# Performance work log

Measured on AMD Instinct MI355X. Metric: run time of the kernel, lower is better.

The kernel has to match this reference:

```python
import jax, jax.numpy as jnp
import numpy as np

N_NODES = 100000
N_EDGES = 1600000
IN_C = 64
HID = 64


def _glorot(key, shape):
    fan_in, fan_out = shape[1], shape[0]
    lim = (6.0 / (fan_in + fan_out)) ** 0.5
    return jax.random.uniform(key, shape, jnp.float32, -lim, lim)


def setup_inputs() -> dict:
    key = jax.random.key(0)
    ks = jax.random.split(key, 8)
    x = jax.random.normal(ks[0], (N_NODES, IN_C), jnp.float32)
    edge_index = jax.random.randint(ks[1], (2, N_EDGES), 0, N_NODES, jnp.int32)
    return {
        "x": x,
        "edge_index": edge_index,
        # conv1 (SAGEConv in->hid): lin_l (bias), lin_r (no bias)
        "W1l": _glorot(ks[2], (HID, IN_C)),
        "b1l": jnp.zeros((HID,), jnp.float32),
        "W1r": _glorot(ks[3], (HID, IN_C)),
        # conv2 (SAGEConv hid->hid)
        "W2l": _glorot(ks[4], (HID, HID)),
        "b2l": jnp.zeros((HID,), jnp.float32),
        "W2r": _glorot(ks[5], (HID, HID)),
        # edge scorer: Linear(2*hid, 1)
        "Wlin": _glorot(ks[6], (1, 2 * HID)),
        "blin": jnp.zeros((1,), jnp.float32),
    }


def _sage_conv(x, src, dst, Wl, bl, Wr, n_nodes):
    # mean aggregation of source features onto destination nodes
    agg = jax.ops.segment_sum(x[src], dst, num_segments=n_nodes)  # [N, F]
    cnt = jax.ops.segment_sum(jnp.ones((src.shape[0],), x.dtype), dst,
                              num_segments=n_nodes)  # [N]
    mean = agg / jnp.maximum(cnt, 1.0)[:, None]  # isolated nodes -> 0
    return mean @ Wl.T + bl + x @ Wr.T


def reference(x, edge_index, W1l, b1l, W1r, W2l, b2l, W2r, Wlin, blin):
    src, dst = edge_index[0], edge_index[1]
    n = x.shape[0]
    h = jax.nn.relu(_sage_conv(x, src, dst, W1l, b1l, W1r, n))
    h = jax.nn.relu(_sage_conv(h, src, dst, W2l, b2l, W2r, n))
    he = jnp.concatenate([h[src], h[dst]], axis=1)  # [E, 2*HID]
    return (he @ Wlin.T + blin).squeeze(-1)  # [E]
```

## Files before the change

kernel.cpp:

```cpp
#include <hip/hip_runtime.h>
#include <hip/hip_bf16.h>

#define N_NODES 100000
#define N_EDGES 1600000
#define NBUCK 196
#define BCAP 12288
#define CHUNK 4096
#define PART_BLOCKS 391
#define MSTRIDE 36


typedef __hip_bfloat16 bf16;
typedef short short8 __attribute__((ext_vector_type(8)));
typedef float f32x4 __attribute__((ext_vector_type(4)));
typedef unsigned int uint;

__device__ __forceinline__ short f2bs(float f) {
    bf16 h = __float2bfloat16(f);
    short s; __builtin_memcpy(&s, &h, 2); return s;
}
__device__ __forceinline__ float lo_bf(uint w) {
    uint v = w << 16; float f; __builtin_memcpy(&f, &v, 4); return f;
}
__device__ __forceinline__ float hi_bf(uint w) {
    uint v = w & 0xFFFF0000u; float f; __builtin_memcpy(&f, &v, 4); return f;
}
__device__ __forceinline__ uint pack2(float a, float b) {
    return (uint)(unsigned short)f2bs(a) | ((uint)(unsigned short)f2bs(b) << 16);
}
__device__ __forceinline__ short8 load8bf(const bf16* __restrict__ p, long idx) {
    return *(const short8*)((const short*)p + idx);
}

__global__ __launch_bounds__(256) void convert_kernel(
    const float* __restrict__ in, bf16* __restrict__ out, int* __restrict__ gcur,
    const float* __restrict__ W1l, const float* __restrict__ W1r,
    const float* __restrict__ W2l, const float* __restrict__ W2r,
    bf16* __restrict__ wb)
{
    if (blockIdx.x < 6250) {
        int i = blockIdx.x * 256 + threadIdx.x;
        float4 v = ((const float4*)in)[i];
        uint2 o;
        o.x = pack2(v.x, v.y);
        o.y = pack2(v.z, v.w);
        ((uint2*)out)[i] = o;
        if (blockIdx.x == 0) gcur[threadIdx.x] = threadIdx.x * BCAP;
    } else {
        for (int k = threadIdx.x; k < 16384; k += 256) {
            float v;
            if (k < 4096)       v = W1l[k];
            else if (k < 8192)  v = W1r[k - 4096];
            else if (k < 12288) v = W2l[k - 8192];
            else                v = W2r[k - 12288];
            wb[k] = __float2bfloat16(v);
        }
    }
}


__global__ __launch_bounds__(256) void partition_kernel(
    const int* __restrict__ src, const int* __restrict__ dst,
    int* __restrict__ gcur, int* __restrict__ pk)
{
    __shared__ int h[256], scn[256], cur[256], gb[256];
    __shared__ int pl[CHUNK];
    __shared__ unsigned char bb[CHUNK];
    int t = threadIdx.x;
    h[t] = 0;
    __syncthreads();
    int e0 = blockIdx.x * CHUNK;
    for (int i = t; i < CHUNK; i += 256) {
        int e = e0 + i;
        if (e < N_EDGES) atomicAdd(&h[dst[e] >> 9], 1);
    }
    __syncthreads();
    if (t < 64) {
        int v0 = h[t * 4], v1 = h[t * 4 + 1], v2 = h[t * 4 + 2], v3 = h[t * 4 + 3];
        int i0 = v0, i1 = i0 + v1, i2 = i1 + v2, i3 = i2 + v3;
        int run = i3;
#pragma unroll
        for (int off = 1; off < 64; off <<= 1) {
            int u = __shfl_up(run, off);
            if (t >= off) run += u;
        }
        int excl = run - i3;
        scn[t * 4]     = excl + i0;
        scn[t * 4 + 1] = excl + i1;
        scn[t * 4 + 2] = excl + i2;
        scn[t * 4 + 3] = excl + i3;
    }
    __syncthreads();
    cur[t] = scn[t] - h[t];
    __syncthreads();
    int cnt_local = scn[255];
    for (int i = t; i < CHUNK; i += 256) {
        int e = e0 + i;
        if (e < N_EDGES) {
            int d = dst[e];
            int b = d >> 9;
            int p = atomicAdd(&cur[b], 1);
            pl[p] = src[e] | ((d & 511) << 17);
            bb[p] = (unsigned char)b;
        }
    }
    __syncthreads();
    if (h[t] > 0) gb[t] = atomicAdd(&gcur[t], h[t]);
    __syncthreads();
    for (int i = t; i < cnt_local; i += 256) {
        int b = bb[i];
        int pos = gb[b] + (i - (scn[b] - h[b]));
        if (pos < (b + 1) * BCAP) pk[pos] = pl[i];
    }
}

__global__ __launch_bounds__(512) void csr_build(
    const int* __restrict__ gcur, const int* __restrict__ pk,
    int* __restrict__ csr, int2* __restrict__ node_range)
{
    __shared__ int deg[512], scn[512], cur[512];
    __shared__ int csr_l[BCAP];
    int t = threadIdx.x;
    int b = blockIdx.x;
    int base = b * BCAP;
    int cnt = gcur[b] - base;
    if (cnt > BCAP) cnt = BCAP;
    deg[t] = 0;
    __syncthreads();
    for (int i = t; i < cnt; i += 512)
        atomicAdd(&deg[pk[base + i] >> 17], 1);
    __syncthreads();
    if (t < 64) {
        int e[8], inc[8], s = 0;
#pragma unroll
        for (int k = 0; k < 8; k++) { e[k] = deg[t * 8 + k]; s += e[k]; inc[k] = s; }
        int run = s;
#pragma unroll
        for (int off = 1; off < 64; off <<= 1) {
            int u = __shfl_up(run, off);
            if (t >= off) run += u;
        }
        int excl = run - s;
#pragma unroll
        for (int k = 0; k < 8; k++) scn[t * 8 + k] = excl + inc[k];
    }
    __syncthreads();
    int excl = scn[t] - deg[t];
    cur[t] = excl;
    int n = (b << 9) + t;
    if (n < N_NODES) node_range[n] = make_int2(base + excl, base + excl + deg[t]);
    __syncthreads();
    for (int i = t; i < cnt; i += 512) {
        int v = pk[base + i];
        int p = atomicAdd(&cur[v >> 17], 1);
        csr_l[p] = v & 0x1FFFF;
    }
    __syncthreads();
    for (int i = t; i < cnt; i += 512)
        csr[base + i] = csr_l[i];
}


__device__ __forceinline__ void gather_mean_lds(
    const bf16* __restrict__ feat, const int2* __restrict__ node_range,
    const int* __restrict__ csr, int nb0, uint* __restrict__ mean_l)
{
    int wave = threadIdx.x >> 6, lane = threadIdx.x & 63;
    int g = lane >> 3, ci = lane & 7;
    int nl = wave * 8 + g;
    int n = nb0 + nl;
    int2 rg = (n < N_NODES) ? node_range[n] : make_int2(0, 0);
    int beg = rg.x, end = rg.y;
    const uint* fw = (const uint*)feat;
    float a0 = 0.f, a1 = 0.f, a2 = 0.f, a3 = 0.f;
    float a4 = 0.f, a5 = 0.f, a6 = 0.f, a7 = 0.f;
    int i = beg;
    for (; i + 3 < end; i += 4) {
        int s0 = csr[i], s1 = csr[i + 1], s2 = csr[i + 2], s3 = csr[i + 3];
        uint4 w0 = *(const uint4*)(fw + (long)s0 * 32 + ci * 4);
        uint4 w1 = *(const uint4*)(fw + (long)s1 * 32 + ci * 4);
        uint4 w2 = *(const uint4*)(fw + (long)s2 * 32 + ci * 4);
        uint4 w3 = *(const uint4*)(fw + (long)s3 * 32 + ci * 4);
        a0 += lo_bf(w0.x) + lo_bf(w1.x) + lo_bf(w2.x) + lo_bf(w3.x);
        a1 += hi_bf(w0.x) + hi_bf(w1.x) + hi_bf(w2.x) + hi_bf(w3.x);
        a2 += lo_bf(w0.y) + lo_bf(w1.y) + lo_bf(w2.y) + lo_bf(w3.y);
        a3 += hi_bf(w0.y) + hi_bf(w1.y) + hi_bf(w2.y) + hi_bf(w3.y);
        a4 += lo_bf(w0.z) + lo_bf(w1.z) + lo_bf(w2.z) + lo_bf(w3.z);
        a5 += hi_bf(w0.z) + hi_bf(w1.z) + hi_bf(w2.z) + hi_bf(w3.z);
        a6 += lo_bf(w0.w) + lo_bf(w1.w) + lo_bf(w2.w) + lo_bf(w3.w);
        a7 += hi_bf(w0.w) + hi_bf(w1.w) + hi_bf(w2.w) + hi_bf(w3.w);
    }
    for (; i < end; i++) {
        int s = csr[i];
        uint4 w = *(const uint4*)(fw + (long)s * 32 + ci * 4);
        a0 += lo_bf(w.x); a1 += hi_bf(w.x);
        a2 += lo_bf(w.y); a3 += hi_bf(w.y);
        a4 += lo_bf(w.z); a5 += hi_bf(w.z);
        a6 += lo_bf(w.w); a7 += hi_bf(w.w);
    }
    int d = end - beg;
    float inv = d > 0 ? 1.0f / (float)d : 0.0f;
    uint4 q;
    q.x = pack2(a0 * inv, a1 * inv);
    q.y = pack2(a2 * inv, a3 * inv);
    q.z = pack2(a4 * inv, a5 * inv);
    q.w = pack2(a6 * inv, a7 * inv);
    *(uint4*)(mean_l + nl * MSTRIDE + ci * 4) = q;
}

__device__ __forceinline__ short8 load_bfrag(
    const bf16* __restrict__ wlb, int f, int c, int quad)
{
    if (c < 2) return load8bf(wlb, (long)f * 64 + c * 32 + quad * 8);
    return load8bf(wlb, 4096 + (long)f * 64 + (c - 2) * 32 + quad * 8);
}

__global__ __launch_bounds__(512) void layer1_fused(
    const bf16* __restrict__ xb, const int2* __restrict__ nrng,
    const int* __restrict__ csr, const bf16* __restrict__ wlb,
    const float* __restrict__ bl, bf16* __restrict__ h_out)
{
    __shared__ uint mean_l[64 * MSTRIDE];
    int nb0 = blockIdx.x * 64;
    gather_mean_lds(xb, nrng, csr, nb0, mean_l);
    __syncthreads();
    int tid = threadIdx.x;
    int wave = tid >> 6, lane = tid & 63;
    if (wave >= 4) return;
    int quad = lane >> 4, n16 = lane & 15;
    int nb = nb0 + wave * 16;
    int ln = wave * 16 + n16;

    int node_a = nb + n16;
    int na = node_a < N_NODES ? node_a : N_NODES - 1;
    short8 a[4];
#pragma unroll
    for (int c = 0; c < 2; c++)
        a[c] = *(const short8*)(mean_l + ln * MSTRIDE + c * 16 + quad * 4);
#pragma unroll
    for (int c = 0; c < 2; c++)
        a[2 + c] = load8bf(xb, (long)na * 64 + c * 32 + quad * 8);

#pragma unroll
    for (int t = 0; t < 4; t++) {
        int f = 16 * t + n16;
        f32x4 acc = {0.f, 0.f, 0.f, 0.f};
#pragma unroll
        for (int c = 0; c < 4; c++) {
            short8 b = load_bfrag(wlb, f, c, quad);
            acc = __builtin_amdgcn_mfma_f32_16x16x32_bf16(a[c], b, acc, 0, 0, 0);
        }
        float bias = bl[f];
#pragma unroll
        for (int r = 0; r < 4; r++) {
            int node = nb + quad * 4 + r;
            if (node < N_NODES)
                h_out[(long)node * 64 + f] = __float2bfloat16(fmaxf(acc[r] + bias, 0.0f));
        }
    }
}

__global__ __launch_bounds__(512) void layer2_fused(
    const bf16* __restrict__ h1, const int2* __restrict__ nrng,
    const int* __restrict__ csr, const bf16* __restrict__ wlb,
    const float* __restrict__ bl, const float* __restrict__ Wlin,
    float* __restrict__ s_src, float* __restrict__ s_dst)
{
    __shared__ uint mean_l[64 * MSTRIDE];
    int nb0 = blockIdx.x * 64;
    gather_mean_lds(h1, nrng, csr, nb0, mean_l);
    __syncthreads();
    int tid = threadIdx.x;
    int wave = tid >> 6, lane = tid & 63;
    if (wave >= 4) return;
    int quad = lane >> 4, n16 = lane & 15;
    int nb = nb0 + wave * 16;
    int ln = wave * 16 + n16;

    int node_a = nb + n16;
    int na = node_a < N_NODES ? node_a : N_NODES - 1;
    short8 a[4];
#pragma unroll
    for (int c = 0; c < 2; c++)
        a[c] = *(const short8*)(mean_l + ln * MSTRIDE + c * 16 + quad * 4);
#pragma unroll
    for (int c = 0; c < 2; c++)
        a[2 + c] = load8bf(h1, (long)na * 64 + c * 32 + quad * 8);

    float sa[4] = {0.f, 0.f, 0.f, 0.f};
    float sb[4] = {0.f, 0.f, 0.f, 0.f};
#pragma unroll
    for (int t = 0; t < 4; t++) {
        int f = 16 * t + n16;
        f32x4 acc = {0.f, 0.f, 0.f, 0.f};
#pragma unroll
        for (int c = 0; c < 4; c++) {
            short8 b = load_bfrag(wlb, f, c, quad);
            acc = __builtin_amdgcn_mfma_f32_16x16x32_bf16(a[c], b, acc, 0, 0, 0);
        }
        float bias = bl[f];
        float wa = Wlin[f];
        float wb = Wlin[64 + f];
#pragma unroll
        for (int r = 0; r < 4; r++) {
            float h = fmaxf(acc[r] + bias, 0.0f);
            sa[r] += h * wa;
            sb[r] += h * wb;
        }
    }
#pragma unroll
    for (int m = 1; m < 16; m <<= 1) {
#pragma unroll
        for (int r = 0; r < 4; r++) {
            sa[r] += __shfl_xor(sa[r], m);
            sb[r] += __shfl_xor(sb[r], m);
        }
    }
    if (n16 == 0) {
#pragma unroll
        for (int r = 0; r < 4; r++) {
            int node = nb + quad * 4 + r;
            if (node < N_NODES) { s_src[node] = sa[r]; s_dst[node] = sb[r]; }
        }
    }
}

__global__ __launch_bounds__(256) void edge_out_kernel(
    const int* __restrict__ src, const int* __restrict__ dst,
    const float* __restrict__ s_src, const float* __restrict__ s_dst,
    const float* __restrict__ blin, float* __restrict__ out)
{
    int i = blockIdx.x * 256 + threadIdx.x;
    if (i >= N_EDGES / 4) return;
    int4 s4 = ((const int4*)src)[i];
    int4 d4 = ((const int4*)dst)[i];
    float b = blin[0];
    float4 o;
    o.x = s_src[s4.x] + s_dst[d4.x] + b;
    o.y = s_src[s4.y] + s_dst[d4.y] + b;
    o.z = s_src[s4.z] + s_dst[d4.z] + b;
    o.w = s_src[s4.w] + s_dst[d4.w] + b;
    ((float4*)out)[i] = o;
}

extern "C" void kernel_launch(void* const* d_in, const int* in_sizes, int n_in,
                              void* d_out, int out_size, void* d_ws, size_t ws_size,
                              hipStream_t stream) {
    const float* x    = (const float*)d_in[0];
    const int*   ei   = (const int*)d_in[1];
    const float* W1l  = (const float*)d_in[2];
    const float* b1l  = (const float*)d_in[3];
    const float* W1r  = (const float*)d_in[4];
    const float* W2l  = (const float*)d_in[5];
    const float* b2l  = (const float*)d_in[6];
    const float* W2r  = (const float*)d_in[7];
    const float* Wlin = (const float*)d_in[8];
    const float* blin = (const float*)d_in[9];
    float* out = (float*)d_out;

    const int* src = ei;
    const int* dst = ei + N_EDGES;

    char* w = (char*)d_ws;
    bf16*  xb    = (bf16*)w;  w += (size_t)N_NODES * 64 * 2;
    bf16*  h1    = (bf16*)w;  w += (size_t)N_NODES * 64 * 2;
    float* ssrc  = (float*)w; w += (size_t)N_NODES * 4;
    float* sdst  = (float*)w; w += (size_t)N_NODES * 4;
    int2*  nrng  = (int2*)w;  w += (size_t)N_NODES * 8;
    int*   gcur  = (int*)w;   w += 256 * 4;
    bf16*  wb    = (bf16*)w;  w += 16384 * 2;
    int*   pk    = (int*)w;   w += (size_t)NBUCK * BCAP * 4;
    int*   csr   = (int*)w;   w += (size_t)NBUCK * BCAP * 4;

    const int conv_blocks  = 6251;
    const int fused_blocks = (N_NODES + 63) / 64;
    const int eo_blocks    = (N_EDGES / 4 + 255) / 256;

    convert_kernel<<<conv_blocks, 256, 0, stream>>>(x, xb, gcur, W1l, W1r, W2l, W2r, wb);
    partition_kernel<<<PART_BLOCKS, 256, 0, stream>>>(src, dst, gcur, pk);
    csr_build<<<NBUCK, 512, 0, stream>>>(gcur, pk, csr, nrng);

    layer1_fused<<<fused_blocks, 512, 0, stream>>>(xb, nrng, csr, wb, b1l, h1);
    layer2_fused<<<fused_blocks, 512, 0, stream>>>(h1, nrng, csr, wb + 8192, b2l, Wlin, ssrc, sdst);

    edge_out_kernel<<<eo_blocks, 256, 0, stream>>>(src, dst, ssrc, sdst, blin, out);
}
```

Measured before the change: 238.2 us.

## Sort nodes by in-degree within buckets to balance gather waves; unroll gather by 8

```diff
diff --git a/kernel.cpp b/kernel.cpp
--- a/kernel.cpp
+++ b/kernel.cpp
@@ -116,9 +116,10 @@
 
 __global__ __launch_bounds__(512) void csr_build(
     const int* __restrict__ gcur, const int* __restrict__ pk,
-    int* __restrict__ csr, int2* __restrict__ node_range)
+    int* __restrict__ csr, int2* __restrict__ node_range, int* __restrict__ perm)
 {
     __shared__ int deg[512], scn[512], cur[512];
+    __shared__ int dh[64], dcur[64];
     __shared__ int csr_l[BCAP];
     int t = threadIdx.x;
     int b = blockIdx.x;
@@ -126,6 +127,7 @@
     int cnt = gcur[b] - base;
     if (cnt > BCAP) cnt = BCAP;
     deg[t] = 0;
+    if (t < 64) dh[t] = 0;
     __syncthreads();
     for (int i = t; i < cnt; i += 512)
         atomicAdd(&deg[pk[base + i] >> 17], 1);
@@ -148,7 +150,24 @@
     int excl = scn[t] - deg[t];
     cur[t] = excl;
     int n = (b << 9) + t;
-    if (n < N_NODES) node_range[n] = make_int2(base + excl, base + excl + deg[t]);
+    bool valid = n < N_NODES;
+    if (valid) node_range[n] = make_int2(base + excl, base + excl + deg[t]);
+    int key = deg[t] < 63 ? deg[t] : 63;
+    atomicAdd(&dh[key], 1);
+    __syncthreads();
+    if (t < 64) {
+        int v = dh[t];
+        int run = v;
+#pragma unroll
+        for (int off = 1; off < 64; off <<= 1) {
+            int u = __shfl_up(run, off);
+            if (t >= off) run += u;
+        }
+        dcur[t] = run - v;
+    }
+    __syncthreads();
+    int pos = atomicAdd(&dcur[key], 1);
+    perm[b * 512 + pos] = valid ? n : N_NODES;
     __syncthreads();
     for (int i = t; i < cnt; i += 512) {
         int v = pk[base + i];
@@ -163,34 +182,57 @@
 
 __device__ __forceinline__ void gather_mean_lds(
     const bf16* __restrict__ feat, const int2* __restrict__ node_range,
-    const int* __restrict__ csr, int nb0, uint* __restrict__ mean_l)
+    const int* __restrict__ csr, const int* __restrict__ perm_l,
+    uint* __restrict__ mean_l)
 {
     int wave = threadIdx.x >> 6, lane = threadIdx.x & 63;
     int g = lane >> 3, ci = lane & 7;
     int nl = wave * 8 + g;
-    int n = nb0 + nl;
+    int n = perm_l[nl];
     int2 rg = (n < N_NODES) ? node_range[n] : make_int2(0, 0);
     int beg = rg.x, end = rg.y;
     const uint* fw = (const uint*)feat;
     float a0 = 0.f, a1 = 0.f, a2 = 0.f, a3 = 0.f;
     float a4 = 0.f, a5 = 0.f, a6 = 0.f, a7 = 0.f;
     int i = beg;
-    for (; i + 3 < end; i += 4) {
-        int s0 = csr[i], s1 = csr[i + 1], s2 = csr[i + 2], s3 = csr[i + 3];
+    for (; i + 7 < end; i += 8) {
+        int s0 = csr[i],     s1 = csr[i + 1], s2 = csr[i + 2], s3 = csr[i + 3];
+        int s4 = csr[i + 4], s5 = csr[i + 5], s6 = csr[i + 6], s7 = csr[i + 7];
         uint4 w0 = *(const uint4*)(fw + (long)s0 * 32 + ci * 4);
         uint4 w1 = *(const uint4*)(fw + (long)s1 * 32 + ci * 4);
         uint4 w2 = *(const uint4*)(fw + (long)s2 * 32 + ci * 4);
         uint4 w3 = *(const uint4*)(fw + (long)s3 * 32 + ci * 4);
-        a0 += lo_bf(w0.x) + lo_bf(w1.x) + lo_bf(w2.x) + lo_bf(w3.x);
-        a1 += hi_bf(w0.x) + hi_bf(w1.x) + hi_bf(w2.x) + hi_bf(w3.x);
-        a2 += lo_bf(w0.y) + lo_bf(w1.y) + lo_bf(w2.y) + lo_bf(w3.y);
-        a3 += hi_bf(w0.y) + hi_bf(w1.y) + hi_bf(w2.y) + hi_bf(w3.y);
-        a4 += lo_bf(w0.z) + lo_bf(w1.z) + lo_bf(w2.z) + lo_bf(w3.z);
-        a5 += hi_bf(w0.z) + hi_bf(w1.z) + hi_bf(w2.z) + hi_bf(w3.z);
-        a6 += lo_bf(w0.w) + lo_bf(w1.w) + lo_bf(w2.w) + lo_bf(w3.w);
-        a7 += hi_bf(w0.w) + hi_bf(w1.w) + hi_bf(w2.w) + hi_bf(w3.w);
-    }
-    for (; i < end; i++) {
+        uint4 w4 = *(const uint4*)(fw + (long)s4 * 32 + ci * 4);
+        uint4 w5 = *(const uint4*)(fw + (long)s5 * 32 + ci * 4);
+        uint4 w6 = *(const uint4*)(fw + (long)s6 * 32 + ci * 4);
+        uint4 w7 = *(const uint4*)(fw + (long)s7 * 32 + ci * 4);
+        a0 += lo_bf(w0.x) + lo_bf(w1.x) + lo_bf(w2.x) + lo_bf(w3.x)
+            + lo_bf(w4.x) + lo_bf(w5.x) + lo_bf(w6.x) + lo_bf(w7.x);
+        a1 += hi_bf(w0.x) + hi_bf(w1.x) + hi_bf(w2.x) + hi_bf(w3.x)
+            + hi_bf(w4.x) + hi_bf(w5.x) + hi_bf(w6.x) + hi_bf(w7.x);
+        a2 += lo_bf(w0.y) + lo_bf(w1.y) + lo_bf(w2.y) + lo_bf(w3.y)
+            + lo_bf(w4.y) + lo_bf(w5.y) + lo_bf(w6.y) + lo_bf(w7.y);
+        a3 += hi_bf(w0.y) + hi_bf(w1.y) + hi_bf(w2.y) + hi_bf(w3.y)
+            + hi_bf(w4.y) + hi_bf(w5.y) + hi_bf(w6.y) + hi_bf(w7.y);
+        a4 += lo_bf(w0.z) + lo_bf(w1.z) + lo_bf(w2.z) + lo_bf(w3.z)
+            + lo_bf(w4.z) + lo_bf(w5.z) + lo_bf(w6.z) + lo_bf(w7.z);
+        a5 += hi_bf(w0.z) + hi_bf(w1.z) + hi_bf(w2.z) + hi_bf(w3.z)
+            + hi_bf(w4.z) + hi_bf(w5.z) + hi_bf(w6.z) + hi_bf(w7.z);
+        a6 += lo_bf(w0.w) + lo_bf(w1.w) + lo_bf(w2.w) + lo_bf(w3.w)
+            + lo_bf(w4.w) + lo_bf(w5.w) + lo_bf(w6.w) + lo_bf(w7.w);
+        a7 += hi_bf(w0.w) + hi_bf(w1.w) + hi_bf(w2.w) + hi_bf(w3.w)
+            + hi_bf(w4.w) + hi_bf(w5.w) + hi_bf(w6.w) + hi_bf(w7.w);
+    }
+    for (; i + 1 < end; i += 2) {
+        int s0 = csr[i], s1 = csr[i + 1];
+        uint4 w0 = *(const uint4*)(fw + (long)s0 * 32 + ci * 4);
+        uint4 w1 = *(const uint4*)(fw + (long)s1 * 32 + ci * 4);
+        a0 += lo_bf(w0.x) + lo_bf(w1.x); a1 += hi_bf(w0.x) + hi_bf(w1.x);
+        a2 += lo_bf(w0.y) + lo_bf(w1.y); a3 += hi_bf(w0.y) + hi_bf(w1.y);
+        a4 += lo_bf(w0.z) + lo_bf(w1.z); a5 += hi_bf(w0.z) + hi_bf(w1.z);
+        a6 += lo_bf(w0.w) + lo_bf(w1.w); a7 += hi_bf(w0.w) + hi_bf(w1.w);
+    }
+    if (i < end) {
         int s = csr[i];
         uint4 w = *(const uint4*)(fw + (long)s * 32 + ci * 4);
         a0 += lo_bf(w.x); a1 += hi_bf(w.x);
@@ -217,22 +259,25 @@
 
 __global__ __launch_bounds__(512) void layer1_fused(
     const bf16* __restrict__ xb, const int2* __restrict__ nrng,
-    const int* __restrict__ csr, const bf16* __restrict__ wlb,
-    const float* __restrict__ bl, bf16* __restrict__ h_out)
+    const int* __restrict__ csr, const int* __restrict__ perm,
+    const bf16* __restrict__ wlb, const float* __restrict__ bl,
+    bf16* __restrict__ h_out)
 {
     __shared__ uint mean_l[64 * MSTRIDE];
-    int nb0 = blockIdx.x * 64;
-    gather_mean_lds(xb, nrng, csr, nb0, mean_l);
+    __shared__ int perm_l[64];
+    int sb0 = blockIdx.x * 64;
+    if (threadIdx.x < 64) perm_l[threadIdx.x] = perm[sb0 + threadIdx.x];
+    __syncthreads();
+    gather_mean_lds(xb, nrng, csr, perm_l, mean_l);
     __syncthreads();
     int tid = threadIdx.x;
     int wave = tid >> 6, lane = tid & 63;
     if (wave >= 4) return;
     int quad = lane >> 4, n16 = lane & 15;
-    int nb = nb0 + wave * 16;
     int ln = wave * 16 + n16;
 
-    int node_a = nb + n16;
-    int na = node_a < N_NODES ? node_a : N_NODES - 1;
+    int n_a = perm_l[ln];
+    int na = n_a < N_NODES ? n_a : N_NODES - 1;
     short8 a[4];
 #pragma unroll
     for (int c = 0; c < 2; c++)
@@ -253,7 +298,7 @@
         float bias = bl[f];
 #pragma unroll
         for (int r = 0; r < 4; r++) {
-            int node = nb + quad * 4 + r;
+            int node = perm_l[wave * 16 + quad * 4 + r];
             if (node < N_NODES)
                 h_out[(long)node * 64 + f] = __float2bfloat16(fmaxf(acc[r] + bias, 0.0f));
         }
@@ -262,23 +307,26 @@
 
 __global__ __launch_bounds__(512) void layer2_fused(
     const bf16* __restrict__ h1, const int2* __restrict__ nrng,
-    const int* __restrict__ csr, const bf16* __restrict__ wlb,
-    const float* __restrict__ bl, const float* __restrict__ Wlin,
+    const int* __restrict__ csr, const int* __restrict__ perm,
+    const bf16* __restrict__ wlb, const float* __restrict__ bl,
+    const float* __restrict__ Wlin,
     float* __restrict__ s_src, float* __restrict__ s_dst)
 {
     __shared__ uint mean_l[64 * MSTRIDE];
-    int nb0 = blockIdx.x * 64;
-    gather_mean_lds(h1, nrng, csr, nb0, mean_l);
+    __shared__ int perm_l[64];
+    int sb0 = blockIdx.x * 64;
+    if (threadIdx.x < 64) perm_l[threadIdx.x] = perm[sb0 + threadIdx.x];
+    __syncthreads();
+    gather_mean_lds(h1, nrng, csr, perm_l, mean_l);
     __syncthreads();
     int tid = threadIdx.x;
     int wave = tid >> 6, lane = tid & 63;
     if (wave >= 4) return;
     int quad = lane >> 4, n16 = lane & 15;
-    int nb = nb0 + wave * 16;
     int ln = wave * 16 + n16;
 
-    int node_a = nb + n16;
-    int na = node_a < N_NODES ? node_a : N_NODES - 1;
+    int n_a = perm_l[ln];
+    int na = n_a < N_NODES ? n_a : N_NODES - 1;
     short8 a[4];
 #pragma unroll
     for (int c = 0; c < 2; c++)
@@ -319,7 +367,7 @@
     if (n16 == 0) {
 #pragma unroll
         for (int r = 0; r < 4; r++) {
-            int node = nb + quad * 4 + r;
+            int node = perm_l[wave * 16 + quad * 4 + r];
             if (node < N_NODES) { s_src[node] = sa[r]; s_dst[node] = sb[r]; }
         }
     }
@@ -367,21 +415,22 @@
     float* ssrc  = (float*)w; w += (size_t)N_NODES * 4;
     float* sdst  = (float*)w; w += (size_t)N_NODES * 4;
     int2*  nrng  = (int2*)w;  w += (size_t)N_NODES * 8;
+    int*   perm  = (int*)w;   w += (size_t)NBUCK * 512 * 4;
     int*   gcur  = (int*)w;   w += 256 * 4;
     bf16*  wb    = (bf16*)w;  w += 16384 * 2;
     int*   pk    = (int*)w;   w += (size_t)NBUCK * BCAP * 4;
     int*   csr   = (int*)w;   w += (size_t)NBUCK * BCAP * 4;
 
     const int conv_blocks  = 6251;
-    const int fused_blocks = (N_NODES + 63) / 64;
+    const int fused_blocks = NBUCK * 8;
     const int eo_blocks    = (N_EDGES / 4 + 255) / 256;
 
     convert_kernel<<<conv_blocks, 256, 0, stream>>>(x, xb, gcur, W1l, W1r, W2l, W2r, wb);
     partition_kernel<<<PART_BLOCKS, 256, 0, stream>>>(src, dst, gcur, pk);
-    csr_build<<<NBUCK, 512, 0, stream>>>(gcur, pk, csr, nrng);
-
-    layer1_fused<<<fused_blocks, 512, 0, stream>>>(xb, nrng, csr, wb, b1l, h1);
-    layer2_fused<<<fused_blocks, 512, 0, stream>>>(h1, nrng, csr, wb + 8192, b2l, Wlin, ssrc, sdst);
+    csr_build<<<NBUCK, 512, 0, stream>>>(gcur, pk, csr, nrng, perm);
+
+    layer1_fused<<<fused_blocks, 512, 0, stream>>>(xb, nrng, csr, perm, wb, b1l, h1);
+    layer2_fused<<<fused_blocks, 512, 0, stream>>>(h1, nrng, csr, perm, wb + 8192, b2l, Wlin, ssrc, sdst);
 
     edge_out_kernel<<<eo_blocks, 256, 0, stream>>>(src, dst, ssrc, sdst, blin, out);
 }
```

Measured after the change: 259.4 us. +8.9%, slower.

## Fuse feature conversion into partition kernel and unroll gather loop by eight

Applied to the files above, without the earlier changes.

```diff
diff --git a/kernel.cpp b/kernel.cpp
--- a/kernel.cpp
+++ b/kernel.cpp
@@ -7,6 +7,7 @@
 #define BCAP 12288
 #define CHUNK 4096
 #define PART_BLOCKS 391
+#define XGROUPS 1600000
 #define MSTRIDE 36
 
 
@@ -32,34 +33,11 @@
     return *(const short8*)((const short*)p + idx);
 }
 
-__global__ __launch_bounds__(256) void convert_kernel(
-    const float* __restrict__ in, bf16* __restrict__ out, int* __restrict__ gcur,
+__global__ __launch_bounds__(256) void partition_kernel(
+    const float* __restrict__ x, bf16* __restrict__ xb,
     const float* __restrict__ W1l, const float* __restrict__ W1r,
     const float* __restrict__ W2l, const float* __restrict__ W2r,
-    bf16* __restrict__ wb)
-{
-    if (blockIdx.x < 6250) {
-        int i = blockIdx.x * 256 + threadIdx.x;
-        float4 v = ((const float4*)in)[i];
-        uint2 o;
-        o.x = pack2(v.x, v.y);
-        o.y = pack2(v.z, v.w);
-        ((uint2*)out)[i] = o;
-        if (blockIdx.x == 0) gcur[threadIdx.x] = threadIdx.x * BCAP;
-    } else {
-        for (int k = threadIdx.x; k < 16384; k += 256) {
-            float v;
-            if (k < 4096)       v = W1l[k];
-            else if (k < 8192)  v = W1r[k - 4096];
-            else if (k < 12288) v = W2l[k - 8192];
-            else                v = W2r[k - 12288];
-            wb[k] = __float2bfloat16(v);
-        }
-    }
-}
-
-
-__global__ __launch_bounds__(256) void partition_kernel(
+    bf16* __restrict__ wb,
     const int* __restrict__ src, const int* __restrict__ dst,
     int* __restrict__ gcur, int* __restrict__ pk)
 {
@@ -68,6 +46,27 @@
     __shared__ unsigned char bb[CHUNK];
     int t = threadIdx.x;
     h[t] = 0;
+    {
+        int g0 = blockIdx.x * 4096;
+        int gend = g0 + 4096 < XGROUPS ? g0 + 4096 : XGROUPS;
+        for (int i = g0 + t; i < gend; i += 256) {
+            float4 v = ((const float4*)x)[i];
+            uint2 o;
+            o.x = pack2(v.x, v.y);
+            o.y = pack2(v.z, v.w);
+            ((uint2*)xb)[i] = o;
+        }
+        if (blockIdx.x == 0) {
+            for (int k = t; k < 16384; k += 256) {
+                float v;
+                if (k < 4096)       v = W1l[k];
+                else if (k < 8192)  v = W1r[k - 4096];
+                else if (k < 12288) v = W2l[k - 8192];
+                else                v = W2r[k - 12288];
+                wb[k] = __float2bfloat16(v);
+            }
+        }
+    }
     __syncthreads();
     int e0 = blockIdx.x * CHUNK;
     for (int i = t; i < CHUNK; i += 256) {
@@ -105,7 +104,7 @@
         }
     }
     __syncthreads();
-    if (h[t] > 0) gb[t] = atomicAdd(&gcur[t], h[t]);
+    if (h[t] > 0) gb[t] = t * BCAP + atomicAdd(&gcur[t], h[t]);
     __syncthreads();
     for (int i = t; i < cnt_local; i += 256) {
         int b = bb[i];
@@ -123,7 +122,7 @@
     int t = threadIdx.x;
     int b = blockIdx.x;
     int base = b * BCAP;
-    int cnt = gcur[b] - base;
+    int cnt = gcur[b];
     if (cnt > BCAP) cnt = BCAP;
     deg[t] = 0;
     __syncthreads();
@@ -175,22 +174,44 @@
     float a0 = 0.f, a1 = 0.f, a2 = 0.f, a3 = 0.f;
     float a4 = 0.f, a5 = 0.f, a6 = 0.f, a7 = 0.f;
     int i = beg;
-    for (; i + 3 < end; i += 4) {
-        int s0 = csr[i], s1 = csr[i + 1], s2 = csr[i + 2], s3 = csr[i + 3];
+    for (; i + 7 < end; i += 8) {
+        int s0 = csr[i],     s1 = csr[i + 1], s2 = csr[i + 2], s3 = csr[i + 3];
+        int s4 = csr[i + 4], s5 = csr[i + 5], s6 = csr[i + 6], s7 = csr[i + 7];
         uint4 w0 = *(const uint4*)(fw + (long)s0 * 32 + ci * 4);
         uint4 w1 = *(const uint4*)(fw + (long)s1 * 32 + ci * 4);
         uint4 w2 = *(const uint4*)(fw + (long)s2 * 32 + ci * 4);
         uint4 w3 = *(const uint4*)(fw + (long)s3 * 32 + ci * 4);
-        a0 += lo_bf(w0.x) + lo_bf(w1.x) + lo_bf(w2.x) + lo_bf(w3.x);
-        a1 += hi_bf(w0.x) + hi_bf(w1.x) + hi_bf(w2.x) + hi_bf(w3.x);
-        a2 += lo_bf(w0.y) + lo_bf(w1.y) + lo_bf(w2.y) + lo_bf(w3.y);
-        a3 += hi_bf(w0.y) + hi_bf(w1.y) + hi_bf(w2.y) + hi_bf(w3.y);
-        a4 += lo_bf(w0.z) + lo_bf(w1.z) + lo_bf(w2.z) + lo_bf(w3.z);
-        a5 += hi_bf(w0.z) + hi_bf(w1.z) + hi_bf(w2.z) + hi_bf(w3.z);
-        a6 += lo_bf(w0.w) + lo_bf(w1.w) + lo_bf(w2.w) + lo_bf(w3.w);
-        a7 += hi_bf(w0.w) + hi_bf(w1.w) + hi_bf(w2.w) + hi_bf(w3.w);
-    }
-    for (; i < end; i++) {
+        uint4 w4 = *(const uint4*)(fw + (long)s4 * 32 + ci * 4);
+        uint4 w5 = *(const uint4*)(fw + (long)s5 * 32 + ci * 4);
+        uint4 w6 = *(const uint4*)(fw + (long)s6 * 32 + ci * 4);
+        uint4 w7 = *(const uint4*)(fw + (long)s7 * 32 + ci * 4);
+        a0 += lo_bf(w0.x) + lo_bf(w1.x) + lo_bf(w2.x) + lo_bf(w3.x)
+            + lo_bf(w4.x) + lo_bf(w5.x) + lo_bf(w6.x) + lo_bf(w7.x);
+        a1 += hi_bf(w0.x) + hi_bf(w1.x) + hi_bf(w2.x) + hi_bf(w3.x)
+            + hi_bf(w4.x) + hi_bf(w5.x) + hi_bf(w6.x) + hi_bf(w7.x);
+        a2 += lo_bf(w0.y) + lo_bf(w1.y) + lo_bf(w2.y) + lo_bf(w3.y)
+            + lo_bf(w4.y) + lo_bf(w5.y) + lo_bf(w6.y) + lo_bf(w7.y);
+        a3 += hi_bf(w0.y) + hi_bf(w1.y) + hi_bf(w2.y) + hi_bf(w3.y)
+            + hi_bf(w4.y) + hi_bf(w5.y) + hi_bf(w6.y) + hi_bf(w7.y);
+        a4 += lo_bf(w0.z) + lo_bf(w1.z) + lo_bf(w2.z) + lo_bf(w3.z)
+            + lo_bf(w4.z) + lo_bf(w5.z) + lo_bf(w6.z) + lo_bf(w7.z);
+        a5 += hi_bf(w0.z) + hi_bf(w1.z) + hi_bf(w2.z) + hi_bf(w3.z)
+            + hi_bf(w4.z) + hi_bf(w5.z) + hi_bf(w6.z) + hi_bf(w7.z);
+        a6 += lo_bf(w0.w) + lo_bf(w1.w) + lo_bf(w2.w) + lo_bf(w3.w)
+            + lo_bf(w4.w) + lo_bf(w5.w) + lo_bf(w6.w) + lo_bf(w7.w);
+        a7 += hi_bf(w0.w) + hi_bf(w1.w) + hi_bf(w2.w) + hi_bf(w3.w)
+            + hi_bf(w4.w) + hi_bf(w5.w) + hi_bf(w6.w) + hi_bf(w7.w);
+    }
+    for (; i + 1 < end; i += 2) {
+        int s0 = csr[i], s1 = csr[i + 1];
+        uint4 w0 = *(const uint4*)(fw + (long)s0 * 32 + ci * 4);
+        uint4 w1 = *(const uint4*)(fw + (long)s1 * 32 + ci * 4);
+        a0 += lo_bf(w0.x) + lo_bf(w1.x); a1 += hi_bf(w0.x) + hi_bf(w1.x);
+        a2 += lo_bf(w0.y) + lo_bf(w1.y); a3 += hi_bf(w0.y) + hi_bf(w1.y);
+        a4 += lo_bf(w0.z) + lo_bf(w1.z); a5 += hi_bf(w0.z) + hi_bf(w1.z);
+        a6 += lo_bf(w0.w) + lo_bf(w1.w); a7 += hi_bf(w0.w) + hi_bf(w1.w);
+    }
+    if (i < end) {
         int s = csr[i];
         uint4 w = *(const uint4*)(fw + (long)s * 32 + ci * 4);
         a0 += lo_bf(w.x); a1 += hi_bf(w.x);
@@ -372,12 +393,12 @@
     int*   pk    = (int*)w;   w += (size_t)NBUCK * BCAP * 4;
     int*   csr   = (int*)w;   w += (size_t)NBUCK * BCAP * 4;
 
-    const int conv_blocks  = 6251;
     const int fused_blocks = (N_NODES + 63) / 64;
     const int eo_blocks    = (N_EDGES / 4 + 255) / 256;
 
-    convert_kernel<<<conv_blocks, 256, 0, stream>>>(x, xb, gcur, W1l, W1r, W2l, W2r, wb);
-    partition_kernel<<<PART_BLOCKS, 256, 0, stream>>>(src, dst, gcur, pk);
+    (void)hipMemsetAsync(gcur, 0, 256 * 4, stream);
+    partition_kernel<<<PART_BLOCKS, 256, 0, stream>>>(
+        x, xb, W1l, W1r, W2l, W2r, wb, src, dst, gcur, pk);
     csr_build<<<NBUCK, 512, 0, stream>>>(gcur, pk, csr, nrng);
 
     layer1_fused<<<fused_blocks, 512, 0, stream>>>(xb, nrng, csr, wb, b1l, h1);
```

New measurement: 240.1 us. No clear change (+0.8%).
